# Kernel tuning notes

Hardware: AMD Instinct MI355X
Metric: run time of the kernel (lower is better)

Reference implementation:

```python
import jax, jax.numpy as jnp
from jax import lax
import numpy as np

N_TOOLS = 50
DIM = 512
N_TOKENS = 8192
PARAM_DIM = 256


def setup_inputs() -> dict:
    key = jax.random.key(0)
    ks = jax.random.split(key, 8)
    s = 1.0 / np.sqrt(DIM)
    x = jax.random.normal(ks[0], (N_TOKENS, DIM), dtype=jnp.float32)
    router_w = jax.random.uniform(ks[1], (N_TOOLS, DIM), jnp.float32, -s, s)
    router_b = jax.random.uniform(ks[2], (N_TOOLS,), jnp.float32, -s, s)
    expert_w = jax.random.uniform(ks[3], (N_TOOLS, DIM, DIM), jnp.float32, -s, s)
    expert_b = jax.random.uniform(ks[4], (N_TOOLS, DIM), jnp.float32, -s, s)
    param_w = jax.random.uniform(ks[5], (PARAM_DIM, DIM), jnp.float32, -s, s)
    param_b = jax.random.uniform(ks[6], (PARAM_DIM,), jnp.float32, -s, s)
    return {"x": x, "router_w": router_w, "router_b": router_b,
            "expert_w": expert_w, "expert_b": expert_b,
            "param_w": param_w, "param_b": param_b}


def _moe_adapt(x, tool_idx, expert_w, expert_b):
    # Top-1 dispatch: for each expert i, y_i = x @ W_i.T + b_i, written only
    # where tool_idx == i. Scan over the fixed 50 experts (mirrors the torch
    # masked per-expert Linear loop) with masked select instead of scatter.
    def step(acc, wb):
        i, W, b = wb
        y = x @ W.T + b  # [N, dim]
        mask = (tool_idx == i)[:, None]
        return jnp.where(mask, y, acc), None

    init = jnp.zeros_like(x)
    acc, _ = lax.scan(step, init, (jnp.arange(N_TOOLS), expert_w, expert_b))
    return acc


def reference(x, router_w, router_b, expert_w, expert_b, param_w, param_b):
    tool_logits = x @ router_w.T + router_b            # [N, 50]
    tool_probs = jax.nn.softmax(tool_logits, axis=-1)   # [N, 50]
    tool_idx = jnp.argmax(tool_probs, axis=-1)          # [N] int
    adapted = _moe_adapt(x, tool_idx, expert_w, expert_b)  # [N, dim]
    params = x @ param_w.T + param_b                    # [N, 256]
    return (tool_idx, tool_probs, adapted, params)
```

## Files before the change

### kernel.cpp

```cpp
#include <hip/hip_runtime.h>
#include <hip/hip_bf16.h>
#include <math.h>

#define N_TOKENS 8192
#define DIM      512
#define N_TOOLS  50
#define PARAM_DIM 256
#define N_ROWBLK (N_TOKENS / 64)
#define MAX_BATCHES 128
#define TM 128
#define LDSS 72

typedef float  f32x4 __attribute__((ext_vector_type(4)));
typedef short  s16x8 __attribute__((ext_vector_type(8)));
typedef short  s16x4 __attribute__((ext_vector_type(4)));

#define WS_IDX     0
#define WS_COUNTS  8192
#define WS_CURSOR  8256
#define WS_OFFSETS 8320
#define WS_BE      8384
#define WS_BM0     8512
#define WS_NB      8640
#define WS_ORDER   8704
#define WS_PWH     16896
#define WS_RWH     82432
#define WS_RWL     98816
#define WS_XH      115200
#define WS_XL      2212352

__device__ inline float bf2f(short s) {
    return __uint_as_float(((unsigned)(unsigned short)s) << 16);
}

__device__ inline s16x4 pk4(float a, float b, float c, float d) {
    __hip_bfloat162 p0 = __float22bfloat162_rn(make_float2(a, b));
    __hip_bfloat162 p1 = __float22bfloat162_rn(make_float2(c, d));
    union { __hip_bfloat162 h; short2 s; } u0, u1;
    u0.h = p0; u1.h = p1;
    s16x4 r; r[0] = u0.s.x; r[1] = u0.s.y; r[2] = u1.s.x; r[3] = u1.s.y;
    return r;
}

#define CVT_XB  4096
#define CVT_PWB 128
#define CVT_RWB 32
#define CVT_GRID (CVT_XB + CVT_PWB + CVT_RWB + 1)
__global__ __launch_bounds__(256) void cvt_kernel(const float* __restrict__ x,
                                                  const float* __restrict__ pw,
                                                  const float* __restrict__ rw,
                                                  short* __restrict__ xh,
                                                  short* __restrict__ xl,
                                                  short* __restrict__ pwh,
                                                  short* __restrict__ rwh,
                                                  short* __restrict__ rwl,
                                                  int* __restrict__ counts) {
    int bid = blockIdx.x;
    int tid = threadIdx.x;
    if (bid < CVT_XB) {
        size_t i = ((size_t)bid * 256 + tid) * 4;
        float4 v = *(const float4*)&x[i];
        s16x4 h = pk4(v.x, v.y, v.z, v.w);
        s16x4 l = pk4(v.x - bf2f(h[0]), v.y - bf2f(h[1]),
                      v.z - bf2f(h[2]), v.w - bf2f(h[3]));
        *(s16x4*)&xh[i] = h;
        *(s16x4*)&xl[i] = l;
    } else if (bid < CVT_XB + CVT_PWB) {
        size_t i = ((size_t)(bid - CVT_XB) * 256 + tid) * 4;
        float4 v = *(const float4*)&pw[i];
        *(s16x4*)&pwh[i] = pk4(v.x, v.y, v.z, v.w);
    } else if (bid < CVT_XB + CVT_PWB + CVT_RWB) {
        int i = ((bid - CVT_XB - CVT_PWB) * 256 + tid) * 4;
        int row = i >> 9;
        float4 v = {0.f, 0.f, 0.f, 0.f};
        if (row < N_TOOLS) v = *(const float4*)&rw[i];
        s16x4 h = pk4(v.x, v.y, v.z, v.w);
        s16x4 l = pk4(v.x - bf2f(h[0]), v.y - bf2f(h[1]),
                      v.z - bf2f(h[2]), v.w - bf2f(h[3]));
        *(s16x4*)&rwh[i] = h;
        *(s16x4*)&rwl[i] = l;
    } else {
        if (tid < 64) counts[tid] = 0;
    }
}

__global__ __launch_bounds__(256) void head_mfma(const short* __restrict__ xh,
                                                 const short* __restrict__ xl,
                                                 const short* __restrict__ pwh,
                                                 const float* __restrict__ pb,
                                                 const short* __restrict__ rwh,
                                                 const short* __restrict__ rwl,
                                                 const float* __restrict__ rb,
                                                 float* __restrict__ out_params,
                                                 float* __restrict__ probs,
                                                 float* __restrict__ out_idx,
                                                 int* __restrict__ idx_i,
                                                 int* __restrict__ counts) {
    int r0 = blockIdx.y * 64;
    bool isl = (blockIdx.x == 4);
    int c0 = isl ? 0 : blockIdx.x * 64;

    __shared__ short As[64 * LDSS];
    __shared__ short Bs[64 * LDSS];
    __shared__ short Al[64 * LDSS];
    __shared__ short Bl[64 * LDSS];
    __shared__ int rowcol[64];

    int tid = threadIdx.x;
    int wv = tid >> 6;
    int lane = tid & 63;
    int fm = lane & 15;
    int q = lane >> 4;

    int ar0 = tid >> 3, ag = tid & 7;
    int ar1 = ar0 + 32;
    const short* aptr0 = xh + (size_t)(r0 + ar0) * DIM + ag * 8;
    const short* aptr1 = xh + (size_t)(r0 + ar1) * DIM + ag * 8;
    const short* alptr0 = xl + (size_t)(r0 + ar0) * DIM + ag * 8;
    const short* alptr1 = xl + (size_t)(r0 + ar1) * DIM + ag * 8;

    const short* bsrc = isl ? rwh : (pwh + (size_t)c0 * DIM);
    int bc[2], bg[2];
    const short* bph[2];
    const short* bpl[2];
#pragma unroll
    for (int i = 0; i < 2; ++i) {
        int u = i * 256 + tid;
        bc[i] = u >> 3; bg[i] = u & 7;
        bph[i] = bsrc + (size_t)bc[i] * DIM + bg[i] * 8;
        bpl[i] = rwl + (size_t)bc[i] * DIM + bg[i] * 8;
    }

    f32x4 acc[4] = {{0.f, 0.f, 0.f, 0.f}, {0.f, 0.f, 0.f, 0.f},
                    {0.f, 0.f, 0.f, 0.f}, {0.f, 0.f, 0.f, 0.f}};

    s16x8 apre0, apre1, alpre0, alpre1;
    s16x8 bpre[2], blpre[2];
    apre0 = *(const s16x8*)aptr0;
    apre1 = *(const s16x8*)aptr1;
    if (isl) { alpre0 = *(const s16x8*)alptr0; alpre1 = *(const s16x8*)alptr1; }
#pragma unroll
    for (int i = 0; i < 2; ++i) {
        bpre[i] = *(const s16x8*)bph[i];
        if (isl) blpre[i] = *(const s16x8*)bpl[i];
    }

    for (int k0 = 0; k0 < DIM; k0 += 64) {
        *(s16x8*)&As[ar0 * LDSS + ag * 8] = apre0;
        *(s16x8*)&As[ar1 * LDSS + ag * 8] = apre1;
#pragma unroll
        for (int i = 0; i < 2; ++i)
            *(s16x8*)&Bs[bc[i] * LDSS + bg[i] * 8] = bpre[i];
        if (isl) {
            *(s16x8*)&Al[ar0 * LDSS + ag * 8] = alpre0;
            *(s16x8*)&Al[ar1 * LDSS + ag * 8] = alpre1;
#pragma unroll
            for (int i = 0; i < 2; ++i)
                *(s16x8*)&Bl[bc[i] * LDSS + bg[i] * 8] = blpre[i];
        }
        __syncthreads();

        int kn = k0 + 64;
        if (kn < DIM) {
            apre0 = *(const s16x8*)(aptr0 + kn);
            apre1 = *(const s16x8*)(aptr1 + kn);
            if (isl) {
                alpre0 = *(const s16x8*)(alptr0 + kn);
                alpre1 = *(const s16x8*)(alptr1 + kn);
            }
#pragma unroll
            for (int i = 0; i < 2; ++i) {
                bpre[i] = *(const s16x8*)(bph[i] + kn);
                if (isl) blpre[i] = *(const s16x8*)(bpl[i] + kn);
            }
        }

#pragma unroll
        for (int kk = 0; kk < 64; kk += 32) {
            int ao = (wv * 16 + fm) * LDSS + kk + q * 8;
            s16x8 a = *(const s16x8*)&As[ao];
            if (!isl) {
#pragma unroll
                for (int n = 0; n < 4; ++n) {
                    s16x8 b = *(const s16x8*)&Bs[(n * 16 + fm) * LDSS + kk + q * 8];
                    acc[n] = __builtin_amdgcn_mfma_f32_16x16x32_bf16(a, b, acc[n], 0, 0, 0);
                }
            } else {
                s16x8 al = *(const s16x8*)&Al[ao];
#pragma unroll
                for (int n = 0; n < 4; ++n) {
                    int bo = (n * 16 + fm) * LDSS + kk + q * 8;
                    s16x8 b  = *(const s16x8*)&Bs[bo];
                    s16x8 bl = *(const s16x8*)&Bl[bo];
                    acc[n] = __builtin_amdgcn_mfma_f32_16x16x32_bf16(a,  b,  acc[n], 0, 0, 0);
                    acc[n] = __builtin_amdgcn_mfma_f32_16x16x32_bf16(a,  bl, acc[n], 0, 0, 0);
                    acc[n] = __builtin_amdgcn_mfma_f32_16x16x32_bf16(al, b,  acc[n], 0, 0, 0);
                }
            }
        }
        __syncthreads();
    }

    if (!isl) {
        float bias[4];
#pragma unroll
        for (int n = 0; n < 4; ++n) bias[n] = pb[c0 + n * 16 + fm];
#pragma unroll
        for (int r = 0; r < 4; ++r) {
            int row = r0 + wv * 16 + q * 4 + r;
            float* op = out_params + (size_t)row * PARAM_DIM + c0;
#pragma unroll
            for (int n = 0; n < 4; ++n) op[n * 16 + fm] = acc[n][r] + bias[n];
        }
    } else {
        float rbv[4];
#pragma unroll
        for (int n = 0; n < 4; ++n) {
            int c = n * 16 + fm;
            rbv[n] = (c < N_TOOLS) ? rb[c] : 0.f;
        }
#pragma unroll
        for (int rr = 0; rr < 4; ++rr) {
            int row_l = wv * 16 + q * 4 + rr;
            int row = r0 + row_l;
            float v[4];
            float vmax = -INFINITY; int vcol = N_TOOLS;
#pragma unroll
            for (int n = 0; n < 4; ++n) {
                int c = n * 16 + fm;
                v[n] = acc[n][rr] + rbv[n];
                if (c < N_TOOLS && v[n] > vmax) { vmax = v[n]; vcol = c; }
            }
#pragma unroll
            for (int s = 1; s < 16; s <<= 1) {
                float om = __shfl_xor(vmax, s, 64);
                int   oc = __shfl_xor(vcol, s, 64);
                if (om > vmax || (om == vmax && oc < vcol)) { vmax = om; vcol = oc; }
            }
            float e[4]; float esum = 0.f;
#pragma unroll
            for (int n = 0; n < 4; ++n) {
                int c = n * 16 + fm;
                e[n] = (c < N_TOOLS) ? expf(v[n] - vmax) : 0.f;
                esum += e[n];
            }
#pragma unroll
            for (int s = 1; s < 16; s <<= 1) esum += __shfl_xor(esum, s, 64);
            float inv = 1.f / esum;
#pragma unroll
            for (int n = 0; n < 4; ++n) {
                int c = n * 16 + fm;
                if (c < N_TOOLS) probs[(size_t)row * N_TOOLS + c] = e[n] * inv;
            }
            if (fm == 0) {
                out_idx[row] = (float)vcol;
                idx_i[row] = vcol;
                rowcol[row_l] = vcol;
            }
        }
        __syncthreads();
        if (wv == 0) {
            int myc = rowcol[lane];
            int cnt = 0;
            for (int e2 = 0; e2 < N_TOOLS; ++e2) {
                unsigned long long m = __ballot(myc == e2);
                if (lane == e2) cnt = __popcll(m);
            }
            if (lane < N_TOOLS && cnt > 0) atomicAdd(&counts[lane], cnt);
        }
    }
}

__global__ void plumb_kernel(const int* __restrict__ counts,
                             int* __restrict__ offsets,
                             int* __restrict__ cursor,
                             int* __restrict__ batch_e,
                             int* __restrict__ batch_m0,
                             int* __restrict__ nb_out) {
    int lane = threadIdx.x;
    int c = (lane < N_TOOLS) ? counts[lane] : 0;
    int pre = c;
#pragma unroll
    for (int s = 1; s < 64; s <<= 1) {
        int v = __shfl_up(pre, s, 64);
        if (lane >= s) pre += v;
    }
    if (lane < N_TOOLS) { offsets[lane] = pre - c; cursor[lane] = pre - c; }

    int nb_i = (lane < N_TOOLS) ? (c + TM - 1) / TM : 0;
    int pre2 = nb_i;
#pragma unroll
    for (int s = 1; s < 64; s <<= 1) {
        int v = __shfl_up(pre2, s, 64);
        if (lane >= s) pre2 += v;
    }
    int bstart = pre2 - nb_i;
    for (int b = 0; b < nb_i; ++b) {
        batch_e[bstart + b] = lane;
        batch_m0[bstart + b] = b * TM;
    }
    if (lane == 63) nb_out[0] = pre2;
}

__global__ __launch_bounds__(256) void reorder_kernel(const int* __restrict__ idx_i,
                                                      int* __restrict__ cursor,
                                                      int* __restrict__ order) {
    __shared__ int lcnt[N_TOOLS];
    __shared__ int lbase[N_TOOLS];
    int tid = threadIdx.x;
    if (tid < N_TOOLS) lcnt[tid] = 0;
    __syncthreads();
    int t = blockIdx.x * 256 + tid;
    int e = idx_i[t];
    int r = atomicAdd(&lcnt[e], 1);
    __syncthreads();
    if (tid < N_TOOLS && lcnt[tid] > 0) lbase[tid] = atomicAdd(&cursor[tid], lcnt[tid]);
    __syncthreads();
    order[lbase[e] + r] = t;
}

__global__ __launch_bounds__(256) void adapted_mfma(const short* __restrict__ xh,
                                                    const float* __restrict__ ew,
                                                    const float* __restrict__ eb,
                                                    const int* __restrict__ order,
                                                    const int* __restrict__ batch_e,
                                                    const int* __restrict__ batch_m0,
                                                    const int* __restrict__ nb_ptr,
                                                    const int* __restrict__ offsets,
                                                    const int* __restrict__ counts,
                                                    float* __restrict__ out) {
    int b = blockIdx.y;
    if (b >= nb_ptr[0]) return;
    int e = batch_e[b];
    int m0 = batch_m0[b];
    int c0 = blockIdx.x * 64;
    int start = offsets[e] + m0;
    int len = counts[e] - m0;
    if (len > TM) len = TM;

    __shared__ short As[TM * LDSS];
    __shared__ short Bs[64 * LDSS];
    __shared__ int toks[TM];

    int tid = threadIdx.x;
    if (tid < TM) toks[tid] = (tid < len) ? order[start + tid] : -1;
    __syncthreads();

    int wv = tid >> 6;
    int lane = tid & 63;
    int fm = lane & 15;
    int q = lane >> 4;

    const float* We = ew + (size_t)e * DIM * DIM;

    int ag = tid & 7;
    int ar[4]; const short* aptr[4];
#pragma unroll
    for (int i = 0; i < 4; ++i) {
        ar[i] = i * 32 + (tid >> 3);
        int tk = toks[ar[i]];
        aptr[i] = (tk >= 0) ? xh + (size_t)tk * DIM + ag * 8 : nullptr;
    }
    int bc[4], bg[4];
    const float* bptr[4];
#pragma unroll
    for (int i = 0; i < 4; ++i) {
        int u = i * 256 + tid;
        bc[i] = u >> 4; bg[i] = u & 15;
        bptr[i] = We + (size_t)(c0 + bc[i]) * DIM + bg[i] * 4;
    }

    f32x4 acc[8] = {{0.f,0.f,0.f,0.f},{0.f,0.f,0.f,0.f},{0.f,0.f,0.f,0.f},{0.f,0.f,0.f,0.f},
                    {0.f,0.f,0.f,0.f},{0.f,0.f,0.f,0.f},{0.f,0.f,0.f,0.f},{0.f,0.f,0.f,0.f}};

    const s16x8 z8 = {0, 0, 0, 0, 0, 0, 0, 0};
    s16x8 apre[4];
    float4 bpre[4];
#pragma unroll
    for (int i = 0; i < 4; ++i) apre[i] = aptr[i] ? *(const s16x8*)aptr[i] : z8;
#pragma unroll
    for (int i = 0; i < 4; ++i) bpre[i] = *(const float4*)bptr[i];

    for (int k0 = 0; k0 < DIM; k0 += 64) {
#pragma unroll
        for (int i = 0; i < 4; ++i)
            *(s16x8*)&As[ar[i] * LDSS + ag * 8] = apre[i];
#pragma unroll
        for (int i = 0; i < 4; ++i) {
            float4 v = bpre[i];
            *(s16x4*)&Bs[bc[i] * LDSS + bg[i] * 4] = pk4(v.x, v.y, v.z, v.w);
        }
        __syncthreads();

        int kn = k0 + 64;
        if (kn < DIM) {
#pragma unroll
            for (int i = 0; i < 4; ++i) apre[i] = aptr[i] ? *(const s16x8*)(aptr[i] + kn) : z8;
#pragma unroll
            for (int i = 0; i < 4; ++i) bpre[i] = *(const float4*)(bptr[i] + kn);
        }

#pragma unroll
        for (int kk = 0; kk < 64; kk += 32) {
            s16x8 a0 = *(const s16x8*)&As[(wv * 32 + fm) * LDSS + kk + q * 8];
            s16x8 a1 = *(const s16x8*)&As[(wv * 32 + 16 + fm) * LDSS + kk + q * 8];
#pragma unroll
            for (int n = 0; n < 4; ++n) {
                s16x8 bf = *(const s16x8*)&Bs[(n * 16 + fm) * LDSS + kk + q * 8];
                acc[n]     = __builtin_amdgcn_mfma_f32_16x16x32_bf16(a0, bf, acc[n],     0, 0, 0);
                acc[4 + n] = __builtin_amdgcn_mfma_f32_16x16x32_bf16(a1, bf, acc[4 + n], 0, 0, 0);
            }
        }
        __syncthreads();
    }

    float bias[4];
#pragma unroll
    for (int n = 0; n < 4; ++n) bias[n] = eb[(size_t)e * DIM + c0 + n * 16 + fm];

#pragma unroll
    for (int m = 0; m < 2; ++m) {
#pragma unroll
        for (int r = 0; r < 4; ++r) {
            int row = wv * 32 + m * 16 + q * 4 + r;
            int tok = toks[row];
            if (tok < 0) continue;
            float* op = out + (size_t)tok * DIM + c0;
#pragma unroll
            for (int n = 0; n < 4; ++n) op[n * 16 + fm] = acc[m * 4 + n][r] + bias[n];
        }
    }
}

extern "C" void kernel_launch(void* const* d_in, const int* in_sizes, int n_in,
                              void* d_out, int out_size, void* d_ws, size_t ws_size,
                              hipStream_t stream) {
    const float* x        = (const float*)d_in[0];
    const float* router_w = (const float*)d_in[1];
    const float* router_b = (const float*)d_in[2];
    const float* expert_w = (const float*)d_in[3];
    const float* expert_b = (const float*)d_in[4];
    const float* param_w  = (const float*)d_in[5];
    const float* param_b  = (const float*)d_in[6];

    float* out = (float*)d_out;
    float* out_idx     = out;
    float* out_probs   = out + N_TOKENS;
    float* out_adapted = out + N_TOKENS + N_TOKENS * N_TOOLS;
    float* out_params  = out_adapted + (size_t)N_TOKENS * DIM;

    int* ws = (int*)d_ws;
    int* ws_idx     = ws + WS_IDX;
    int* ws_counts  = ws + WS_COUNTS;
    int* ws_cursor  = ws + WS_CURSOR;
    int* ws_offsets = ws + WS_OFFSETS;
    int* ws_be      = ws + WS_BE;
    int* ws_bm0     = ws + WS_BM0;
    int* ws_nb      = ws + WS_NB;
    int* ws_order   = ws + WS_ORDER;
    short* ws_pwh   = (short*)(ws + WS_PWH);
    short* ws_rwh   = (short*)(ws + WS_RWH);
    short* ws_rwl   = (short*)(ws + WS_RWL);
    short* ws_xh    = (short*)(ws + WS_XH);
    short* ws_xl    = (short*)(ws + WS_XL);

    cvt_kernel<<<CVT_GRID, 256, 0, stream>>>(x, param_w, router_w,
                                             ws_xh, ws_xl, ws_pwh, ws_rwh, ws_rwl,
                                             ws_counts);

    head_mfma<<<dim3(5, N_ROWBLK), 256, 0, stream>>>(ws_xh, ws_xl, ws_pwh, param_b,
                                                     ws_rwh, ws_rwl, router_b,
                                                     out_params, out_probs,
                                                     out_idx, ws_idx, ws_counts);

    plumb_kernel<<<1, 64, 0, stream>>>(ws_counts, ws_offsets, ws_cursor,
                                       ws_be, ws_bm0, ws_nb);

    reorder_kernel<<<N_TOKENS / 256, 256, 0, stream>>>(ws_idx, ws_cursor, ws_order);

    adapted_mfma<<<dim3(8, MAX_BATCHES), 256, 0, stream>>>(ws_xh, expert_w, expert_b,
                                                           ws_order, ws_be, ws_bm0, ws_nb,
                                                           ws_offsets, ws_counts, out_adapted);
}
```

Before: 152.3 us.

## Double expert GEMM row tile to 256 and swizzle block order for weight reuse

The per-expert GEMM tile grows from 128 to 256 token rows, so each wave computes 64 rows (16 accumulators) and each converted weight tile is reused across twice as many tokens. This cuts redundant fp32 weight loads and bf16 conversion per expert. The grid becomes 1D with a swizzle that groups 8 batches per column tile so neighbouring blocks share weight columns in cache. Fewer, larger blocks and more registers per thread may lower occupancy and leave CUs idle when experts have few tokens.

```diff
diff --git a/kernel.cpp b/kernel.cpp
--- a/kernel.cpp
+++ b/kernel.cpp
@@ -7,8 +7,8 @@
 #define N_TOOLS  50
 #define PARAM_DIM 256
 #define N_ROWBLK (N_TOKENS / 64)
-#define MAX_BATCHES 128
-#define TM 128
+#define MAX_BATCHES 96
+#define TM 256
 #define LDSS 72
 
 typedef float  f32x4 __attribute__((ext_vector_type(4)));
@@ -329,11 +329,13 @@
                                                     const int* __restrict__ offsets,
                                                     const int* __restrict__ counts,
                                                     float* __restrict__ out) {
-    int b = blockIdx.y;
+    int bid = blockIdx.x;
+    int b = ((bid >> 6) << 3) + (bid & 7);
+    int ct = (bid >> 3) & 7;
     if (b >= nb_ptr[0]) return;
     int e = batch_e[b];
     int m0 = batch_m0[b];
-    int c0 = blockIdx.x * 64;
+    int c0 = ct * 64;
     int start = offsets[e] + m0;
     int len = counts[e] - m0;
     if (len > TM) len = TM;
@@ -343,7 +345,7 @@
     __shared__ int toks[TM];
 
     int tid = threadIdx.x;
-    if (tid < TM) toks[tid] = (tid < len) ? order[start + tid] : -1;
+    toks[tid] = (tid < len) ? order[start + tid] : -1;
     __syncthreads();
 
     int wv = tid >> 6;
@@ -354,37 +356,38 @@
     const float* We = ew + (size_t)e * DIM * DIM;
 
     int ag = tid & 7;
-    int ar[4]; const short* aptr[4];
-#pragma unroll
-    for (int i = 0; i < 4; ++i) {
-        ar[i] = i * 32 + (tid >> 3);
-        int tk = toks[ar[i]];
+    int arr = tid >> 3;
+    const short* aptr[8];
+#pragma unroll
+    for (int i = 0; i < 8; ++i) {
+        int tk = toks[i * 32 + arr];
         aptr[i] = (tk >= 0) ? xh + (size_t)tk * DIM + ag * 8 : nullptr;
     }
     int bc[4], bg[4];
     const float* bptr[4];
 #pragma unroll
     for (int i = 0; i < 4; ++i) {
-        int u = i * 256 + tid;
-        bc[i] = u >> 4; bg[i] = u & 15;
+        int u2 = i * 256 + tid;
+        bc[i] = u2 >> 4; bg[i] = u2 & 15;
         bptr[i] = We + (size_t)(c0 + bc[i]) * DIM + bg[i] * 4;
     }
 
-    f32x4 acc[8] = {{0.f,0.f,0.f,0.f},{0.f,0.f,0.f,0.f},{0.f,0.f,0.f,0.f},{0.f,0.f,0.f,0.f},
-                    {0.f,0.f,0.f,0.f},{0.f,0.f,0.f,0.f},{0.f,0.f,0.f,0.f},{0.f,0.f,0.f,0.f}};
+    f32x4 acc[16];
+#pragma unroll
+    for (int i = 0; i < 16; ++i) acc[i] = (f32x4){0.f, 0.f, 0.f, 0.f};
 
     const s16x8 z8 = {0, 0, 0, 0, 0, 0, 0, 0};
-    s16x8 apre[4];
+    s16x8 apre[8];
     float4 bpre[4];
 #pragma unroll
-    for (int i = 0; i < 4; ++i) apre[i] = aptr[i] ? *(const s16x8*)aptr[i] : z8;
+    for (int i = 0; i < 8; ++i) apre[i] = aptr[i] ? *(const s16x8*)aptr[i] : z8;
 #pragma unroll
     for (int i = 0; i < 4; ++i) bpre[i] = *(const float4*)bptr[i];
 
     for (int k0 = 0; k0 < DIM; k0 += 64) {
 #pragma unroll
-        for (int i = 0; i < 4; ++i)
-            *(s16x8*)&As[ar[i] * LDSS + ag * 8] = apre[i];
+        for (int i = 0; i < 8; ++i)
+            *(s16x8*)&As[(i * 32 + arr) * LDSS + ag * 8] = apre[i];
 #pragma unroll
         for (int i = 0; i < 4; ++i) {
             float4 v = bpre[i];
@@ -395,20 +398,23 @@
         int kn = k0 + 64;
         if (kn < DIM) {
 #pragma unroll
-            for (int i = 0; i < 4; ++i) apre[i] = aptr[i] ? *(const s16x8*)(aptr[i] + kn) : z8;
+            for (int i = 0; i < 8; ++i) apre[i] = aptr[i] ? *(const s16x8*)(aptr[i] + kn) : z8;
 #pragma unroll
             for (int i = 0; i < 4; ++i) bpre[i] = *(const float4*)(bptr[i] + kn);
         }
 
 #pragma unroll
         for (int kk = 0; kk < 64; kk += 32) {
-            s16x8 a0 = *(const s16x8*)&As[(wv * 32 + fm) * LDSS + kk + q * 8];
-            s16x8 a1 = *(const s16x8*)&As[(wv * 32 + 16 + fm) * LDSS + kk + q * 8];
+            s16x8 a[4];
+#pragma unroll
+            for (int m = 0; m < 4; ++m)
+                a[m] = *(const s16x8*)&As[(wv * 64 + m * 16 + fm) * LDSS + kk + q * 8];
 #pragma unroll
             for (int n = 0; n < 4; ++n) {
-                s16x8 bf = *(const s16x8*)&Bs[(n * 16 + fm) * LDSS + kk + q * 8];
-                acc[n]     = __builtin_amdgcn_mfma_f32_16x16x32_bf16(a0, bf, acc[n],     0, 0, 0);
-                acc[4 + n] = __builtin_amdgcn_mfma_f32_16x16x32_bf16(a1, bf, acc[4 + n], 0, 0, 0);
+                s16x8 bfv = *(const s16x8*)&Bs[(n * 16 + fm) * LDSS + kk + q * 8];
+#pragma unroll
+                for (int m = 0; m < 4; ++m)
+                    acc[n * 4 + m] = __builtin_amdgcn_mfma_f32_16x16x32_bf16(a[m], bfv, acc[n * 4 + m], 0, 0, 0);
             }
         }
         __syncthreads();
@@ -419,15 +425,15 @@
     for (int n = 0; n < 4; ++n) bias[n] = eb[(size_t)e * DIM + c0 + n * 16 + fm];
 
 #pragma unroll
-    for (int m = 0; m < 2; ++m) {
+    for (int m = 0; m < 4; ++m) {
 #pragma unroll
         for (int r = 0; r < 4; ++r) {
-            int row = wv * 32 + m * 16 + q * 4 + r;
+            int row = wv * 64 + m * 16 + q * 4 + r;
             int tok = toks[row];
             if (tok < 0) continue;
             float* op = out + (size_t)tok * DIM + c0;
 #pragma unroll
-            for (int n = 0; n < 4; ++n) op[n * 16 + fm] = acc[m * 4 + n][r] + bias[n];
+            for (int n = 0; n < 4; ++n) op[n * 16 + fm] = acc[n * 4 + m][r] + bias[n];
         }
     }
 }
@@ -478,7 +484,7 @@
 
     reorder_kernel<<<N_TOKENS / 256, 256, 0, stream>>>(ws_idx, ws_cursor, ws_order);
 
-    adapted_mfma<<<dim3(8, MAX_BATCHES), 256, 0, stream>>>(ws_xh, expert_w, expert_b,
-                                                           ws_order, ws_be, ws_bm0, ws_nb,
-                                                           ws_offsets, ws_counts, out_adapted);
-}
+    adapted_mfma<<<768, 256, 0, stream>>>(ws_xh, expert_w, expert_b,
+                                          ws_order, ws_be, ws_bm0, ws_nb,
+                                          ws_offsets, ws_counts, out_adapted);
+}
```

Result: slower. 157.2 us (+3.2%).

## Fuse pipeline into one cooperative persistent kernel with grid syncs

Applied to the files above, without the earlier changes.

Replaces the five separate launches (convert, head GEMM, plumbing, reorder, expert GEMM) with a single cooperative kernel of 512 persistent blocks that step through the stages separated by grid-wide syncs. The per-expert batch table is recomputed inside each block from counts, which removes the single-thread plumb kernel. The goal is to remove launch gaps and tail idle time between stages. In exchange it relies on cooperative launch co-residency at 2 blocks per CU and adds grid-barrier cost, and it keeps the multi-kernel path as a fallback if the cooperative launch fails.

```diff
diff --git a/kernel.cpp b/kernel.cpp
--- a/kernel.cpp
+++ b/kernel.cpp
@@ -1,15 +1,26 @@
 #include <hip/hip_runtime.h>
+#include <hip/hip_cooperative_groups.h>
 #include <hip/hip_bf16.h>
 #include <math.h>
+
+namespace cg = cooperative_groups;
 
 #define N_TOKENS 8192
 #define DIM      512
 #define N_TOOLS  50
 #define PARAM_DIM 256
 #define N_ROWBLK (N_TOKENS / 64)
-#define MAX_BATCHES 128
 #define TM 128
+#define MAXB 192
 #define LDSS 72
+#define TILE_SH (64 * LDSS)
+#define GRID 512
+#define NHEAD 640
+
+#define CVT_XB  4096
+#define CVT_PWB 128
+#define CVT_RWB 32
+#define CVT_UNITS (CVT_XB + CVT_PWB + CVT_RWB + 1)
 
 typedef float  f32x4 __attribute__((ext_vector_type(4)));
 typedef short  s16x8 __attribute__((ext_vector_type(8)));
@@ -20,14 +31,14 @@
 #define WS_CURSOR  8256
 #define WS_OFFSETS 8320
 #define WS_BE      8384
-#define WS_BM0     8512
-#define WS_NB      8640
-#define WS_ORDER   8704
-#define WS_PWH     16896
-#define WS_RWH     82432
-#define WS_RWL     98816
-#define WS_XH      115200
-#define WS_XL      2212352
+#define WS_BM0     8576
+#define WS_NB      8768
+#define WS_ORDER   8784
+#define WS_PWH     16976
+#define WS_RWH     82512
+#define WS_RWL     98896
+#define WS_XH      115280
+#define WS_XL      2212432
 
 __device__ inline float bf2f(short s) {
     return __uint_as_float(((unsigned)(unsigned short)s) << 16);
@@ -42,10 +53,369 @@
     return r;
 }
 
-#define CVT_XB  4096
-#define CVT_PWB 128
-#define CVT_RWB 32
-#define CVT_GRID (CVT_XB + CVT_PWB + CVT_RWB + 1)
+__global__ __launch_bounds__(256, 2) void mega(
+        const float* __restrict__ x,
+        const float* __restrict__ rw, const float* __restrict__ rb,
+        const float* __restrict__ ew, const float* __restrict__ eb,
+        const float* __restrict__ pw, const float* __restrict__ pbias,
+        float* __restrict__ out_idx, float* __restrict__ probs,
+        float* __restrict__ out_adapted, float* __restrict__ out_params,
+        int* __restrict__ idx_i, int* __restrict__ counts,
+        int* __restrict__ cursor, int* __restrict__ order,
+        short* __restrict__ pwh, short* __restrict__ rwh, short* __restrict__ rwl,
+        short* __restrict__ xh, short* __restrict__ xl) {
+    cg::grid_group gg = cg::this_grid();
+    __shared__ short smem[4 * TILE_SH];
+    __shared__ int misc[256];
+    int bid = blockIdx.x;
+    int tid = threadIdx.x;
+    int wv = tid >> 6;
+    int lane = tid & 63;
+    int fm = lane & 15;
+    int q = lane >> 4;
+
+    for (int u = bid; u < CVT_UNITS; u += GRID) {
+        if (u < CVT_XB) {
+            size_t i = ((size_t)u * 256 + tid) * 4;
+            float4 v = *(const float4*)&x[i];
+            s16x4 h = pk4(v.x, v.y, v.z, v.w);
+            s16x4 l = pk4(v.x - bf2f(h[0]), v.y - bf2f(h[1]),
+                          v.z - bf2f(h[2]), v.w - bf2f(h[3]));
+            *(s16x4*)&xh[i] = h;
+            *(s16x4*)&xl[i] = l;
+        } else if (u < CVT_XB + CVT_PWB) {
+            size_t i = ((size_t)(u - CVT_XB) * 256 + tid) * 4;
+            float4 v = *(const float4*)&pw[i];
+            *(s16x4*)&pwh[i] = pk4(v.x, v.y, v.z, v.w);
+        } else if (u < CVT_XB + CVT_PWB + CVT_RWB) {
+            int i = ((u - CVT_XB - CVT_PWB) * 256 + tid) * 4;
+            int row = i >> 9;
+            float4 v = {0.f, 0.f, 0.f, 0.f};
+            if (row < N_TOOLS) v = *(const float4*)&rw[i];
+            s16x4 h = pk4(v.x, v.y, v.z, v.w);
+            s16x4 l = pk4(v.x - bf2f(h[0]), v.y - bf2f(h[1]),
+                          v.z - bf2f(h[2]), v.w - bf2f(h[3]));
+            *(s16x4*)&rwh[i] = h;
+            *(s16x4*)&rwl[i] = l;
+        } else {
+            if (tid < 64) { counts[tid] = 0; cursor[tid] = 0; }
+        }
+    }
+    __threadfence();
+    gg.sync();
+
+    {
+        short* As = smem;
+        short* Bs = smem + TILE_SH;
+        short* Al = smem + 2 * TILE_SH;
+        short* Bl = smem + 3 * TILE_SH;
+        for (int u = bid; u < NHEAD; u += GRID) {
+            int tl = u % 5;
+            int yy = u / 5;
+            int r0 = yy * 64;
+            bool isl = (tl == 4);
+            int c0 = isl ? 0 : tl * 64;
+
+            int ar0 = tid >> 3, ag = tid & 7;
+            int ar1 = ar0 + 32;
+            const short* aptr0 = xh + (size_t)(r0 + ar0) * DIM + ag * 8;
+            const short* aptr1 = xh + (size_t)(r0 + ar1) * DIM + ag * 8;
+            const short* alptr0 = xl + (size_t)(r0 + ar0) * DIM + ag * 8;
+            const short* alptr1 = xl + (size_t)(r0 + ar1) * DIM + ag * 8;
+
+            const short* bsrc = isl ? rwh : (pwh + (size_t)c0 * DIM);
+            int bc[2], bg[2];
+            const short* bph[2];
+            const short* bpl[2];
+#pragma unroll
+            for (int i = 0; i < 2; ++i) {
+                int u2 = i * 256 + tid;
+                bc[i] = u2 >> 3; bg[i] = u2 & 7;
+                bph[i] = bsrc + (size_t)bc[i] * DIM + bg[i] * 8;
+                bpl[i] = rwl + (size_t)bc[i] * DIM + bg[i] * 8;
+            }
+
+            f32x4 acc[4] = {{0.f, 0.f, 0.f, 0.f}, {0.f, 0.f, 0.f, 0.f},
+                            {0.f, 0.f, 0.f, 0.f}, {0.f, 0.f, 0.f, 0.f}};
+
+            s16x8 apre0, apre1, alpre0, alpre1;
+            s16x8 bpre[2], blpre[2];
+            apre0 = *(const s16x8*)aptr0;
+            apre1 = *(const s16x8*)aptr1;
+            if (isl) { alpre0 = *(const s16x8*)alptr0; alpre1 = *(const s16x8*)alptr1; }
+#pragma unroll
+            for (int i = 0; i < 2; ++i) {
+                bpre[i] = *(const s16x8*)bph[i];
+                if (isl) blpre[i] = *(const s16x8*)bpl[i];
+            }
+
+            for (int k0 = 0; k0 < DIM; k0 += 64) {
+                *(s16x8*)&As[ar0 * LDSS + ag * 8] = apre0;
+                *(s16x8*)&As[ar1 * LDSS + ag * 8] = apre1;
+#pragma unroll
+                for (int i = 0; i < 2; ++i)
+                    *(s16x8*)&Bs[bc[i] * LDSS + bg[i] * 8] = bpre[i];
+                if (isl) {
+                    *(s16x8*)&Al[ar0 * LDSS + ag * 8] = alpre0;
+                    *(s16x8*)&Al[ar1 * LDSS + ag * 8] = alpre1;
+#pragma unroll
+                    for (int i = 0; i < 2; ++i)
+                        *(s16x8*)&Bl[bc[i] * LDSS + bg[i] * 8] = blpre[i];
+                }
+                __syncthreads();
+
+                int kn = k0 + 64;
+                if (kn < DIM) {
+                    apre0 = *(const s16x8*)(aptr0 + kn);
+                    apre1 = *(const s16x8*)(aptr1 + kn);
+                    if (isl) {
+                        alpre0 = *(const s16x8*)(alptr0 + kn);
+                        alpre1 = *(const s16x8*)(alptr1 + kn);
+                    }
+#pragma unroll
+                    for (int i = 0; i < 2; ++i) {
+                        bpre[i] = *(const s16x8*)(bph[i] + kn);
+                        if (isl) blpre[i] = *(const s16x8*)(bpl[i] + kn);
+                    }
+                }
+
+#pragma unroll
+                for (int kk = 0; kk < 64; kk += 32) {
+                    int ao = (wv * 16 + fm) * LDSS + kk + q * 8;
+                    s16x8 a = *(const s16x8*)&As[ao];
+                    if (!isl) {
+#pragma unroll
+                        for (int n = 0; n < 4; ++n) {
+                            s16x8 b = *(const s16x8*)&Bs[(n * 16 + fm) * LDSS + kk + q * 8];
+                            acc[n] = __builtin_amdgcn_mfma_f32_16x16x32_bf16(a, b, acc[n], 0, 0, 0);
+                        }
+                    } else {
+                        s16x8 al = *(const s16x8*)&Al[ao];
+#pragma unroll
+                        for (int n = 0; n < 4; ++n) {
+                            int bo = (n * 16 + fm) * LDSS + kk + q * 8;
+                            s16x8 b  = *(const s16x8*)&Bs[bo];
+                            s16x8 bl = *(const s16x8*)&Bl[bo];
+                            acc[n] = __builtin_amdgcn_mfma_f32_16x16x32_bf16(a,  b,  acc[n], 0, 0, 0);
+                            acc[n] = __builtin_amdgcn_mfma_f32_16x16x32_bf16(a,  bl, acc[n], 0, 0, 0);
+                            acc[n] = __builtin_amdgcn_mfma_f32_16x16x32_bf16(al, b,  acc[n], 0, 0, 0);
+                        }
+                    }
+                }
+                __syncthreads();
+            }
+
+            if (!isl) {
+                float bias[4];
+#pragma unroll
+                for (int n = 0; n < 4; ++n) bias[n] = pbias[c0 + n * 16 + fm];
+#pragma unroll
+                for (int r = 0; r < 4; ++r) {
+                    int row = r0 + wv * 16 + q * 4 + r;
+                    float* op = out_params + (size_t)row * PARAM_DIM + c0;
+#pragma unroll
+                    for (int n = 0; n < 4; ++n) op[n * 16 + fm] = acc[n][r] + bias[n];
+                }
+            } else {
+                float rbv[4];
+#pragma unroll
+                for (int n = 0; n < 4; ++n) {
+                    int c = n * 16 + fm;
+                    rbv[n] = (c < N_TOOLS) ? rb[c] : 0.f;
+                }
+#pragma unroll
+                for (int rr = 0; rr < 4; ++rr) {
+                    int row_l = wv * 16 + q * 4 + rr;
+                    int row = r0 + row_l;
+                    float v[4];
+                    float vmax = -INFINITY; int vcol = N_TOOLS;
+#pragma unroll
+                    for (int n = 0; n < 4; ++n) {
+                        int c = n * 16 + fm;
+                        v[n] = acc[n][rr] + rbv[n];
+                        if (c < N_TOOLS && v[n] > vmax) { vmax = v[n]; vcol = c; }
+                    }
+#pragma unroll
+                    for (int s = 1; s < 16; s <<= 1) {
+                        float om = __shfl_xor(vmax, s, 64);
+                        int   oc = __shfl_xor(vcol, s, 64);
+                        if (om > vmax || (om == vmax && oc < vcol)) { vmax = om; vcol = oc; }
+                    }
+                    float e[4]; float esum = 0.f;
+#pragma unroll
+                    for (int n = 0; n < 4; ++n) {
+                        int c = n * 16 + fm;
+                        e[n] = (c < N_TOOLS) ? expf(v[n] - vmax) : 0.f;
+                        esum += e[n];
+                    }
+#pragma unroll
+                    for (int s = 1; s < 16; s <<= 1) esum += __shfl_xor(esum, s, 64);
+                    float inv = 1.f / esum;
+#pragma unroll
+                    for (int n = 0; n < 4; ++n) {
+                        int c = n * 16 + fm;
+                        if (c < N_TOOLS) probs[(size_t)row * N_TOOLS + c] = e[n] * inv;
+                    }
+                    if (fm == 0) {
+                        out_idx[row] = (float)vcol;
+                        idx_i[row] = vcol;
+                        misc[row_l] = vcol;
+                    }
+                }
+                __syncthreads();
+                if (wv == 0) {
+                    int myc = misc[lane];
+                    int cnt = 0;
+                    for (int e2 = 0; e2 < N_TOOLS; ++e2) {
+                        unsigned long long m = __ballot(myc == e2);
+                        if (lane == e2) cnt = __popcll(m);
+                    }
+                    if (lane < N_TOOLS && cnt > 0) atomicAdd(&counts[lane], cnt);
+                }
+            }
+            __syncthreads();
+        }
+    }
+    __threadfence();
+    gg.sync();
+
+    for (int u = bid; u < N_TOKENS / 256; u += GRID) {
+        if (tid < N_TOOLS) misc[tid] = 0;
+        if (wv == 1) {
+            int c = (lane < N_TOOLS) ? counts[lane] : 0;
+            int pre = c;
+#pragma unroll
+            for (int s = 1; s < 64; s <<= 1) {
+                int v = __shfl_up(pre, s, 64);
+                if (lane >= s) pre += v;
+            }
+            misc[64 + lane] = pre - c;
+        }
+        __syncthreads();
+        int t = u * 256 + tid;
+        int e = idx_i[t];
+        int r = atomicAdd(&misc[e], 1);
+        __syncthreads();
+        if (tid < N_TOOLS) {
+            int c2 = misc[tid];
+            misc[128 + tid] = (c2 > 0) ? atomicAdd(&cursor[tid], c2) : 0;
+        }
+        __syncthreads();
+        order[misc[64 + e] + misc[128 + e] + r] = t;
+        __syncthreads();
+    }
+    __threadfence();
+    gg.sync();
+
+    {
+        short* As = smem;
+        short* Bs = smem + 2 * TILE_SH;
+        for (int u = bid; u < MAXB * 8; u += GRID) {
+            int b = u >> 3;
+            int ct = u & 7;
+            __syncthreads();
+            if (tid < 64) misc[128 + tid] = (tid < N_TOOLS) ? counts[tid] : 0;
+            __syncthreads();
+            int e = -1, m0 = 0, off = 0;
+            int accb = 0, acco = 0;
+            for (int i = 0; i < N_TOOLS; ++i) {
+                int c = misc[128 + i];
+                int nb = (c + TM - 1) >> 7;
+                if (e < 0 && b < accb + nb) { e = i; m0 = (b - accb) * TM; off = acco; }
+                accb += nb; acco += c;
+            }
+            if (e < 0) continue;
+            int c0 = ct * 64;
+            int start = off + m0;
+            int len = misc[128 + e] - m0;
+            if (len > TM) len = TM;
+
+            if (tid < TM) misc[tid] = (tid < len) ? order[start + tid] : -1;
+            __syncthreads();
+
+            const float* We = ew + (size_t)e * DIM * DIM;
+
+            int ag = tid & 7;
+            int ar[4]; const short* aptr[4];
+#pragma unroll
+            for (int i = 0; i < 4; ++i) {
+                ar[i] = i * 32 + (tid >> 3);
+                int tk = misc[ar[i]];
+                aptr[i] = (tk >= 0) ? xh + (size_t)tk * DIM + ag * 8 : nullptr;
+            }
+            int bc[4], bg[4];
+            const float* bptr[4];
+#pragma unroll
+            for (int i = 0; i < 4; ++i) {
+                int u2 = i * 256 + tid;
+                bc[i] = u2 >> 4; bg[i] = u2 & 15;
+                bptr[i] = We + (size_t)(c0 + bc[i]) * DIM + bg[i] * 4;
+            }
+
+            f32x4 acc[8] = {{0.f,0.f,0.f,0.f},{0.f,0.f,0.f,0.f},{0.f,0.f,0.f,0.f},{0.f,0.f,0.f,0.f},
+                            {0.f,0.f,0.f,0.f},{0.f,0.f,0.f,0.f},{0.f,0.f,0.f,0.f},{0.f,0.f,0.f,0.f}};
+
+            const s16x8 z8 = {0, 0, 0, 0, 0, 0, 0, 0};
+            s16x8 apre[4];
+            float4 bpre[4];
+#pragma unroll
+            for (int i = 0; i < 4; ++i) apre[i] = aptr[i] ? *(const s16x8*)aptr[i] : z8;
+#pragma unroll
+            for (int i = 0; i < 4; ++i) bpre[i] = *(const float4*)bptr[i];
+
+            for (int k0 = 0; k0 < DIM; k0 += 64) {
+#pragma unroll
+                for (int i = 0; i < 4; ++i)
+                    *(s16x8*)&As[ar[i] * LDSS + ag * 8] = apre[i];
+#pragma unroll
+                for (int i = 0; i < 4; ++i) {
+                    float4 v = bpre[i];
+                    *(s16x4*)&Bs[bc[i] * LDSS + bg[i] * 4] = pk4(v.x, v.y, v.z, v.w);
+                }
+                __syncthreads();
+
+                int kn = k0 + 64;
+                if (kn < DIM) {
+#pragma unroll
+                    for (int i = 0; i < 4; ++i) apre[i] = aptr[i] ? *(const s16x8*)(aptr[i] + kn) : z8;
+#pragma unroll
+                    for (int i = 0; i < 4; ++i) bpre[i] = *(const float4*)(bptr[i] + kn);
+                }
+
+#pragma unroll
+                for (int kk = 0; kk < 64; kk += 32) {
+                    s16x8 a0 = *(const s16x8*)&As[(wv * 32 + fm) * LDSS + kk + q * 8];
+                    s16x8 a1 = *(const s16x8*)&As[(wv * 32 + 16 + fm) * LDSS + kk + q * 8];
+#pragma unroll
+                    for (int n = 0; n < 4; ++n) {
+                        s16x8 bf = *(const s16x8*)&Bs[(n * 16 + fm) * LDSS + kk + q * 8];
+                        acc[n]     = __builtin_amdgcn_mfma_f32_16x16x32_bf16(a0, bf, acc[n],     0, 0, 0);
+                        acc[4 + n] = __builtin_amdgcn_mfma_f32_16x16x32_bf16(a1, bf, acc[4 + n], 0, 0, 0);
+                    }
+                }
+                __syncthreads();
+            }
+
+            float bias[4];
+#pragma unroll
+            for (int n = 0; n < 4; ++n) bias[n] = eb[(size_t)e * DIM + c0 + n * 16 + fm];
+
+#pragma unroll
+            for (int m = 0; m < 2; ++m) {
+#pragma unroll
+                for (int r = 0; r < 4; ++r) {
+                    int row = wv * 32 + m * 16 + q * 4 + r;
+                    int tok = misc[row];
+                    if (tok < 0) continue;
+                    float* op = out_adapted + (size_t)tok * DIM + c0;
+#pragma unroll
+                    for (int n = 0; n < 4; ++n) op[n * 16 + fm] = acc[m * 4 + n][r] + bias[n];
+                }
+            }
+        }
+    }
+}
+
 __global__ __launch_bounds__(256) void cvt_kernel(const float* __restrict__ x,
                                                   const float* __restrict__ pw,
                                                   const float* __restrict__ rw,
@@ -464,21 +834,29 @@
     short* ws_xh    = (short*)(ws + WS_XH);
     short* ws_xl    = (short*)(ws + WS_XL);
 
-    cvt_kernel<<<CVT_GRID, 256, 0, stream>>>(x, param_w, router_w,
-                                             ws_xh, ws_xl, ws_pwh, ws_rwh, ws_rwl,
-                                             ws_counts);
-
-    head_mfma<<<dim3(5, N_ROWBLK), 256, 0, stream>>>(ws_xh, ws_xl, ws_pwh, param_b,
-                                                     ws_rwh, ws_rwl, router_b,
-                                                     out_params, out_probs,
-                                                     out_idx, ws_idx, ws_counts);
-
-    plumb_kernel<<<1, 64, 0, stream>>>(ws_counts, ws_offsets, ws_cursor,
-                                       ws_be, ws_bm0, ws_nb);
-
-    reorder_kernel<<<N_TOKENS / 256, 256, 0, stream>>>(ws_idx, ws_cursor, ws_order);
-
-    adapted_mfma<<<dim3(8, MAX_BATCHES), 256, 0, stream>>>(ws_xh, expert_w, expert_b,
-                                                           ws_order, ws_be, ws_bm0, ws_nb,
-                                                           ws_offsets, ws_counts, out_adapted);
+    void* args[] = {
+        (void*)&x, (void*)&router_w, (void*)&router_b,
+        (void*)&expert_w, (void*)&expert_b,
+        (void*)&param_w, (void*)&param_b,
+        (void*)&out_idx, (void*)&out_probs, (void*)&out_adapted, (void*)&out_params,
+        (void*)&ws_idx, (void*)&ws_counts, (void*)&ws_cursor, (void*)&ws_order,
+        (void*)&ws_pwh, (void*)&ws_rwh, (void*)&ws_rwl, (void*)&ws_xh, (void*)&ws_xl
+    };
+    hipError_t err = hipLaunchCooperativeKernel((void*)mega, dim3(GRID), dim3(256),
+                                                args, 0, stream);
+    if (err != hipSuccess) {
+        cvt_kernel<<<CVT_UNITS, 256, 0, stream>>>(x, param_w, router_w,
+                                                  ws_xh, ws_xl, ws_pwh, ws_rwh, ws_rwl,
+                                                  ws_counts);
+        head_mfma<<<dim3(5, N_ROWBLK), 256, 0, stream>>>(ws_xh, ws_xl, ws_pwh, param_b,
+                                                         ws_rwh, ws_rwl, router_b,
+                                                         out_params, out_probs,
+                                                         out_idx, ws_idx, ws_counts);
+        plumb_kernel<<<1, 64, 0, stream>>>(ws_counts, ws_offsets, ws_cursor,
+                                           ws_be, ws_bm0, ws_nb);
+        reorder_kernel<<<N_TOKENS / 256, 256, 0, stream>>>(ws_idx, ws_cursor, ws_order);
+        adapted_mfma<<<dim3(8, MAXB), 256, 0, stream>>>(ws_xh, expert_w, expert_b,
+                                                        ws_order, ws_be, ws_bm0, ws_nb,
+                                                        ws_offsets, ws_counts, out_adapted);
+    }
 }
```

After: 459.8 us. 202% more time.
